# Kernel optimization log

Hardware: AMD Instinct MI355X
Metric: run time of the kernel (lower is better)

The kernel has to match this reference:

```python
import jax, jax.numpy as jnp
import numpy as np

B, S, H, D = 4, 2048, 16, 128

def setup_inputs() -> dict:
    key = jax.random.key(0)
    kq, kk, kv = jax.random.split(key, 3)
    shape = (B, S, H, D)
    return {
        "q": jax.random.normal(kq, shape, dtype=jnp.float32),
        "k": jax.random.normal(kk, shape, dtype=jnp.float32),
        "v": jax.random.normal(kv, shape, dtype=jnp.float32),
    }

def reference(q, k, v):
    # Fused recurrent linear attention (causal, unnormalized):
    #   H_t = H_{t-1} + k_t v_t^T ;  o_t = (scale * q_t) @ H_t
    scale = jnp.asarray(q.shape[-1], q.dtype) ** -0.5
    # move seq axis to front for scan: [S, B, H, D]
    qs = jnp.moveaxis(q, 1, 0) * scale
    ks = jnp.moveaxis(k, 1, 0)
    vs = jnp.moveaxis(v, 1, 0)

    def step(h, qkv):
        qt, kt, vt = qkv  # each [B, H, D]
        h = h + kt[..., :, None] * vt[..., None, :]  # [B, H, Dk, Dv]
        o = jnp.einsum('bhk,bhkv->bhv', qt, h)       # [B, H, Dv]
        return h, o

    h0 = jnp.zeros((q.shape[0], q.shape[2], q.shape[3], v.shape[3]), dtype=q.dtype)
    _, o = jax.lax.scan(step, h0, (qs, ks, vs))
    return jnp.moveaxis(o, 0, 1)  # [B, S, H, D]
```

## Files before the change

### kernel.cpp

```cpp
#include <hip/hip_runtime.h>


#define Bc 4
#define Sq 2048
#define Hh 16
#define Dd 128
#define RS (Hh * Dd)
#define Cc 128
#define NCH (Sq / Cc)
#define BHt (Bc * Hh)
#define NSEG 4
#define CPS (NCH / NSEG)
#define SCALE 0.08838834764831845f

using frag_ab = __attribute__((ext_vector_type(8))) short;
using frag_cd = __attribute__((ext_vector_type(4))) float;

__device__ __forceinline__ unsigned short f2bf(float f) {
  union { float f; unsigned u; } x; x.f = f;
  unsigned r = x.u + 0x7FFFu + ((x.u >> 16) & 1u);
  return (unsigned short)(r >> 16);
}
__device__ __forceinline__ float bf2f(unsigned short u) {
  union { unsigned u; float f; } x; x.u = ((unsigned)u) << 16;
  return x.f;
}
__device__ __forceinline__ int sw64(int r, int c) {
  return r * 64 + ((((c >> 3) ^ (r & 7)) << 3) | (c & 7));
}
__device__ __forceinline__ int sw128(int r, int c) {
  return r * 128 + ((((c >> 3) ^ (r & 15)) << 3) | (c & 7));
}
__device__ __forceinline__ int swKT(int dk, int t) {
  return dk * 128 + ((((t >> 3) ^ (dk ^ (dk >> 4))) & 15) << 3) + (t & 7);
}
__device__ __forceinline__ int swVT(int dv, int t) {
  return dv * 128 + ((((t >> 3) ^ dv) & 15) << 3) + (t & 7);
}

__global__ __launch_bounds__(256) void phA_state(const float* __restrict__ kg,
                                                 const float* __restrict__ vg,
                                                 unsigned short* __restrict__ st) {
  __shared__ unsigned short KT[128 * 128];
  __shared__ unsigned short VT[16 * 128];
  const int tid = threadIdx.x;
  const int bh = blockIdx.x & 63;
  const int slice = (blockIdx.x >> 6) & 7;
  const int seg = blockIdx.x >> 9;
  const int b = bh >> 4, h = bh & 15;
  const int dv0 = slice * 16;
  const size_t base = (size_t)b * Sq * RS + (size_t)h * Dd;
  const int w = tid >> 6, L = tid & 63, li = L & 15, q4 = L >> 4;
  const int kdk0 = (tid & 31) * 4;
  const int ktg4 = (tid >> 5) * 4;
  const int vdv0l = (tid & 3) * 4;
  const int vt0 = (tid >> 2) * 2;

  float4 rk[4][4];
  float4 rv[2];
  auto prefetch = [&](int n) {
    const size_t t0g = (size_t)n * Cc;
#pragma unroll
    for (int p = 0; p < 4; ++p) {
      const int t0 = p * 32 + ktg4;
#pragma unroll
      for (int i = 0; i < 4; ++i)
        rk[p][i] = *(const float4*)(kg + base + (t0g + t0 + i) * (size_t)RS + kdk0);
    }
#pragma unroll
    for (int i = 0; i < 2; ++i)
      rv[i] = *(const float4*)(vg + base + (t0g + vt0 + i) * (size_t)RS + dv0 + vdv0l);
  };

  frag_cd acc[2];
  acc[0] = (frag_cd){0.f, 0.f, 0.f, 0.f};
  acc[1] = (frag_cd){0.f, 0.f, 0.f, 0.f};
  const int n0 = seg * CPS;
  prefetch(n0);
  const size_t sbb = (size_t)bh * NCH * (128 * 128);

  auto store_acc = [&](int slot) {
    const size_t sb = sbb + (size_t)slot * (128 * 128);
#pragma unroll
    for (int nt = 0; nt < 2; ++nt)
#pragma unroll
      for (int r = 0; r < 4; ++r) {
        const int dv = dv0 + 4 * q4 + r;
        const int dk = 32 * w + 16 * nt + li;
        st[sb + (size_t)dv * 128 + dk] = f2bf(acc[nt][r]);
      }
  };

  for (int j = 0; j < CPS; ++j) {
    __syncthreads();
#pragma unroll
    for (int p = 0; p < 4; ++p) {
      const int t0 = p * 32 + ktg4;
#pragma unroll
      for (int jj = 0; jj < 4; ++jj) {
        ushort4 u;
        u.x = f2bf(((const float*)&rk[p][0])[jj]);
        u.y = f2bf(((const float*)&rk[p][1])[jj]);
        u.z = f2bf(((const float*)&rk[p][2])[jj]);
        u.w = f2bf(((const float*)&rk[p][3])[jj]);
        *(ushort4*)&KT[swKT(kdk0 + jj, t0)] = u;
      }
    }
#pragma unroll
    for (int jj = 0; jj < 4; ++jj) {
      ushort2 u;
      u.x = f2bf(((const float*)&rv[0])[jj]);
      u.y = f2bf(((const float*)&rv[1])[jj]);
      *(ushort2*)&VT[swVT(vdv0l + jj, vt0)] = u;
    }
    if (j + 1 < CPS) prefetch(n0 + j + 1);
    __syncthreads();
    if (j > 0) store_acc(n0 + j);
#pragma unroll
    for (int kt = 0; kt < 4; ++kt) {
      frag_ab af = *(const frag_ab*)&VT[swVT(li, 32 * kt + 8 * q4)];
#pragma unroll
      for (int nt = 0; nt < 2; ++nt) {
        frag_ab bf = *(const frag_ab*)&KT[swKT(32 * w + 16 * nt + li, 32 * kt + 8 * q4)];
        acc[nt] = __builtin_amdgcn_mfma_f32_16x16x32_bf16(af, bf, acc[nt], 0, 0, 0);
      }
    }
  }
  if (seg + 1 < NSEG) store_acc(n0);
}

__global__ __launch_bounds__(256) void phB_out(const float* __restrict__ qg,
                                               const float* __restrict__ kg,
                                               const float* __restrict__ vg,
                                               const unsigned short* __restrict__ st,
                                               float* __restrict__ o) {
  __shared__ unsigned short QP[128 * 128];
  __shared__ unsigned short Bb[128 * 64];
  const int tid = threadIdx.x;
  const int bid = blockIdx.x;
  const int bh = bid & 63, n = bid >> 6;
  const int b = bh >> 4, h = bh & 15;
  const size_t cbase = (size_t)b * Sq * RS + (size_t)n * Cc * RS + (size_t)h * Dd;
  const size_t sbh = (size_t)bh * NCH * (128 * 128);
  const int sseg = n >> 2, jj = n & 3;
  const int nmat = sseg + (jj ? 1 : 0);
  const int w = tid >> 6, L = tid & 63;
  const int wr = w >> 1, wc = w & 1, li = L & 15, q4 = L >> 4;

#pragma unroll
  for (int it = 0; it < 16; ++it) {
    const int f = it * 256 + tid;
    const int t = f >> 5;
    const int c0 = (f & 31) << 2;
    const float4 q4v = *(const float4*)(qg + cbase + (size_t)t * RS + c0);
    ushort4 qu;
    qu.x = f2bf(q4v.x * SCALE); qu.y = f2bf(q4v.y * SCALE);
    qu.z = f2bf(q4v.z * SCALE); qu.w = f2bf(q4v.w * SCALE);
    *(ushort4*)&QP[sw128(t, c0)] = qu;
  }
  frag_cd accO[4][4], accP[4][4];
#pragma unroll
  for (int i = 0; i < 4; ++i)
#pragma unroll
    for (int j = 0; j < 4; ++j) {
      accO[i][j] = (frag_cd){0.f, 0.f, 0.f, 0.f};
      accP[i][j] = (frag_cd){0.f, 0.f, 0.f, 0.f};
    }

  if (nmat > 0) {
    for (int half = 0; half < 2; ++half) {
      __syncthreads();
      if (nmat == 1) {
        const int slot = sseg ? 0 : n;
#pragma unroll
        for (int it = 0; it < 4; ++it) {
          const int f = it * 256 + tid;
          const int dv = f >> 3;
          const int c8 = (f & 7) << 3;
          const uint4 hv = *(const uint4*)(st + sbh + ((size_t)slot << 14) +
                                           (size_t)dv * 128 + 64 * half + c8);
          *(uint4*)&Bb[sw64(dv, c8)] = hv;
        }
      } else {
#pragma unroll
        for (int it = 0; it < 4; ++it) {
          const int f = it * 256 + tid;
          const int dv = f >> 3;
          const int c8 = (f & 7) << 3;
          float s8[8];
#pragma unroll
          for (int e = 0; e < 8; ++e) s8[e] = 0.f;
          for (int m = 0; m < nmat; ++m) {
            const int slot = (m < sseg) ? (m << 2) : n;
            const uint4 hv = *(const uint4*)(st + sbh + ((size_t)slot << 14) +
                                             (size_t)dv * 128 + 64 * half + c8);
            const unsigned hw[4] = {hv.x, hv.y, hv.z, hv.w};
#pragma unroll
            for (int e = 0; e < 4; ++e) {
              s8[2 * e + 0] += bf2f((unsigned short)(hw[e] & 0xFFFFu));
              s8[2 * e + 1] += bf2f((unsigned short)(hw[e] >> 16));
            }
          }
          unsigned pk[4];
#pragma unroll
          for (int e = 0; e < 4; ++e)
            pk[e] = (unsigned)f2bf(s8[2 * e]) | ((unsigned)f2bf(s8[2 * e + 1]) << 16);
          uint4 hv; hv.x = pk[0]; hv.y = pk[1]; hv.z = pk[2]; hv.w = pk[3];
          *(uint4*)&Bb[sw64(dv, c8)] = hv;
        }
      }
      __syncthreads();
#pragma unroll
      for (int kt = 0; kt < 2; ++kt) {
        const int ktg = 2 * half + kt;
        frag_ab af[4], bf_[4];
#pragma unroll
        for (int mt = 0; mt < 4; ++mt)
          af[mt] = *(const frag_ab*)&QP[sw128(64 * wr + 16 * mt + li, 32 * ktg + 8 * q4)];
#pragma unroll
        for (int nt = 0; nt < 4; ++nt)
          bf_[nt] = *(const frag_ab*)&Bb[sw64(64 * wc + 16 * nt + li, 32 * kt + 8 * q4)];
#pragma unroll
        for (int mt = 0; mt < 4; ++mt)
#pragma unroll
          for (int nt = 0; nt < 4; ++nt)
            accO[mt][nt] = __builtin_amdgcn_mfma_f32_16x16x32_bf16(af[mt], bf_[nt], accO[mt][nt], 0, 0, 0);
      }
    }
  }

  for (int half = 0; half < 2; ++half) {
    __syncthreads();
#pragma unroll
    for (int it = 0; it < 8; ++it) {
      const int f = it * 256 + tid;
      const int t = f >> 4;
      const int c0 = (f & 15) << 2;
      const float4 k4v = *(const float4*)(kg + cbase + (size_t)t * RS + 64 * half + c0);
      ushort4 ku;
      ku.x = f2bf(k4v.x); ku.y = f2bf(k4v.y); ku.z = f2bf(k4v.z); ku.w = f2bf(k4v.w);
      *(ushort4*)&Bb[sw64(t, c0)] = ku;
    }
    __syncthreads();
    if (64 * wc <= 64 * wr + 63) {
#pragma unroll
      for (int kt = 0; kt < 2; ++kt) {
        const int ktg = 2 * half + kt;
        frag_ab af[4], bf_[4];
#pragma unroll
        for (int mt = 0; mt < 4; ++mt)
          af[mt] = *(const frag_ab*)&QP[sw128(64 * wr + 16 * mt + li, 32 * ktg + 8 * q4)];
#pragma unroll
        for (int nt = 0; nt < 4; ++nt)
          bf_[nt] = *(const frag_ab*)&Bb[sw64(64 * wc + 16 * nt + li, 32 * kt + 8 * q4)];
#pragma unroll
        for (int mt = 0; mt < 4; ++mt)
#pragma unroll
          for (int nt = 0; nt < 4; ++nt)
            if (64 * wc + 16 * nt <= 64 * wr + 16 * mt + 15)
              accP[mt][nt] = __builtin_amdgcn_mfma_f32_16x16x32_bf16(af[mt], bf_[nt], accP[mt][nt], 0, 0, 0);
      }
    }
  }
  __syncthreads();
#pragma unroll
  for (int mt = 0; mt < 4; ++mt)
#pragma unroll
    for (int nt = 0; nt < 4; ++nt) {
      const int t0 = 64 * wr + 16 * mt + 4 * q4;
      const int s = 64 * wc + 16 * nt + li;
#pragma unroll
      for (int r = 0; r < 4; ++r) {
        const int t = t0 + r;
        QP[sw128(t, s)] = (s <= t) ? f2bf(accP[mt][nt][r]) : (unsigned short)0;
      }
    }

  for (int half = 0; half < 2; ++half) {
    __syncthreads();
#pragma unroll
    for (int it = 0; it < 8; ++it) {
      const int sl = (tid & 15) | ((it & 3) << 4);
      const int c0 = ((tid >> 4) | ((it >> 2) << 4)) << 2;
      const int s = 64 * half + sl;
      const float4 v4v = *(const float4*)(vg + cbase + (size_t)s * RS + c0);
      Bb[sw64(c0 + 0, sl)] = f2bf(v4v.x);
      Bb[sw64(c0 + 1, sl)] = f2bf(v4v.y);
      Bb[sw64(c0 + 2, sl)] = f2bf(v4v.z);
      Bb[sw64(c0 + 3, sl)] = f2bf(v4v.w);
    }
    __syncthreads();
#pragma unroll
    for (int kt = 0; kt < 2; ++kt) {
      const int ktg = 2 * half + kt;
      if (32 * ktg > 64 * wr + 63) continue;
      frag_ab af[4], bf_[4];
#pragma unroll
      for (int mt = 0; mt < 4; ++mt)
        af[mt] = *(const frag_ab*)&QP[sw128(64 * wr + 16 * mt + li, 32 * ktg + 8 * q4)];
#pragma unroll
      for (int nt = 0; nt < 4; ++nt)
        bf_[nt] = *(const frag_ab*)&Bb[sw64(64 * wc + 16 * nt + li, 32 * kt + 8 * q4)];
#pragma unroll
      for (int mt = 0; mt < 4; ++mt)
#pragma unroll
        for (int nt = 0; nt < 4; ++nt)
          if (32 * ktg <= 64 * wr + 16 * mt + 15)
            accO[mt][nt] = __builtin_amdgcn_mfma_f32_16x16x32_bf16(af[mt], bf_[nt], accO[mt][nt], 0, 0, 0);
    }
  }
#pragma unroll
  for (int mt = 0; mt < 4; ++mt)
#pragma unroll
    for (int nt = 0; nt < 4; ++nt)
#pragma unroll
      for (int r = 0; r < 4; ++r) {
        const int t = 64 * wr + 16 * mt + 4 * q4 + r;
        const int dv = 64 * wc + 16 * nt + li;
        o[cbase + (size_t)t * RS + dv] = accO[mt][nt][r];
      }
}

extern "C" void kernel_launch(void* const* d_in, const int* in_sizes, int n_in,
                              void* d_out, int out_size, void* d_ws, size_t ws_size,
                              hipStream_t stream) {
  const float* q = (const float*)d_in[0];
  const float* k = (const float*)d_in[1];
  const float* v = (const float*)d_in[2];
  float* o = (float*)d_out;
  unsigned short* st = (unsigned short*)d_ws;
  hipLaunchKernelGGL(phA_state, dim3(BHt * 8 * NSEG), dim3(256), 0, stream, k, v, st);
  hipLaunchKernelGGL(phB_out, dim3(BHt * NCH), dim3(256), 0, stream, q, k, v, st, o);
}
```

Measured before the change: 289.4 us.

## Split phB output chunk into two 64-row query tiles per block

Each phB block now handles 64 query rows of a 128-token chunk instead of 128, doubling the grid and halving the accumulator registers and Q shared memory. A launch-bounds occupancy hint of 4 blocks per CU is added. The first tile skips loading the later K rows and the second half of V because of causality. The cost is that the inter-chunk state matrix and the K/V data are loaded and converted twice per chunk, once by each tile block.

```diff
diff --git a/kernel.cpp b/kernel.cpp
--- a/kernel.cpp
+++ b/kernel.cpp
@@ -129,18 +129,19 @@
   if (seg + 1 < NSEG) store_acc(n0);
 }
 
-__global__ __launch_bounds__(256) void phB_out(const float* __restrict__ qg,
-                                               const float* __restrict__ kg,
-                                               const float* __restrict__ vg,
-                                               const unsigned short* __restrict__ st,
-                                               float* __restrict__ o) {
-  __shared__ unsigned short QP[128 * 128];
+__global__ __launch_bounds__(256, 4) void phB_out(const float* __restrict__ qg,
+                                                  const float* __restrict__ kg,
+                                                  const float* __restrict__ vg,
+                                                  const unsigned short* __restrict__ st,
+                                                  float* __restrict__ o) {
+  __shared__ unsigned short QP[64 * 128];
   __shared__ unsigned short Bb[128 * 64];
   const int tid = threadIdx.x;
   const int bid = blockIdx.x;
-  const int bh = bid & 63, n = bid >> 6;
+  const int bh = bid & 63, n = (bid >> 6) & 15, tb = bid >> 10;
   const int b = bh >> 4, h = bh & 15;
   const size_t cbase = (size_t)b * Sq * RS + (size_t)n * Cc * RS + (size_t)h * Dd;
+  const size_t tbase = cbase + (size_t)(64 * tb) * RS;
   const size_t sbh = (size_t)bh * NCH * (128 * 128);
   const int sseg = n >> 2, jj = n & 3;
   const int nmat = sseg + (jj ? 1 : 0);
@@ -148,19 +149,19 @@
   const int wr = w >> 1, wc = w & 1, li = L & 15, q4 = L >> 4;
 
 #pragma unroll
-  for (int it = 0; it < 16; ++it) {
+  for (int it = 0; it < 8; ++it) {
     const int f = it * 256 + tid;
     const int t = f >> 5;
     const int c0 = (f & 31) << 2;
-    const float4 q4v = *(const float4*)(qg + cbase + (size_t)t * RS + c0);
+    const float4 q4v = *(const float4*)(qg + tbase + (size_t)t * RS + c0);
     ushort4 qu;
     qu.x = f2bf(q4v.x * SCALE); qu.y = f2bf(q4v.y * SCALE);
     qu.z = f2bf(q4v.z * SCALE); qu.w = f2bf(q4v.w * SCALE);
     *(ushort4*)&QP[sw128(t, c0)] = qu;
   }
-  frag_cd accO[4][4], accP[4][4];
-#pragma unroll
-  for (int i = 0; i < 4; ++i)
+  frag_cd accO[2][4], accP[2][4];
+#pragma unroll
+  for (int i = 0; i < 2; ++i)
 #pragma unroll
     for (int j = 0; j < 4; ++j) {
       accO[i][j] = (frag_cd){0.f, 0.f, 0.f, 0.f};
@@ -213,15 +214,15 @@
 #pragma unroll
       for (int kt = 0; kt < 2; ++kt) {
         const int ktg = 2 * half + kt;
-        frag_ab af[4], bf_[4];
-#pragma unroll
-        for (int mt = 0; mt < 4; ++mt)
-          af[mt] = *(const frag_ab*)&QP[sw128(64 * wr + 16 * mt + li, 32 * ktg + 8 * q4)];
+        frag_ab af[2], bf_[4];
+#pragma unroll
+        for (int mt = 0; mt < 2; ++mt)
+          af[mt] = *(const frag_ab*)&QP[sw128(32 * wr + 16 * mt + li, 32 * ktg + 8 * q4)];
 #pragma unroll
         for (int nt = 0; nt < 4; ++nt)
           bf_[nt] = *(const frag_ab*)&Bb[sw64(64 * wc + 16 * nt + li, 32 * kt + 8 * q4)];
 #pragma unroll
-        for (int mt = 0; mt < 4; ++mt)
+        for (int mt = 0; mt < 2; ++mt)
 #pragma unroll
           for (int nt = 0; nt < 4; ++nt)
             accO[mt][nt] = __builtin_amdgcn_mfma_f32_16x16x32_bf16(af[mt], bf_[nt], accO[mt][nt], 0, 0, 0);
@@ -231,52 +232,66 @@
 
   for (int half = 0; half < 2; ++half) {
     __syncthreads();
-#pragma unroll
-    for (int it = 0; it < 8; ++it) {
-      const int f = it * 256 + tid;
-      const int t = f >> 4;
-      const int c0 = (f & 15) << 2;
-      const float4 k4v = *(const float4*)(kg + cbase + (size_t)t * RS + 64 * half + c0);
-      ushort4 ku;
-      ku.x = f2bf(k4v.x); ku.y = f2bf(k4v.y); ku.z = f2bf(k4v.z); ku.w = f2bf(k4v.w);
-      *(ushort4*)&Bb[sw64(t, c0)] = ku;
-    }
-    __syncthreads();
-    if (64 * wc <= 64 * wr + 63) {
+    if (tb) {
+#pragma unroll
+      for (int it = 0; it < 8; ++it) {
+        const int f = it * 256 + tid;
+        const int t = f >> 4;
+        const int c0 = (f & 15) << 2;
+        const float4 k4v = *(const float4*)(kg + cbase + (size_t)t * RS + 64 * half + c0);
+        ushort4 ku;
+        ku.x = f2bf(k4v.x); ku.y = f2bf(k4v.y); ku.z = f2bf(k4v.z); ku.w = f2bf(k4v.w);
+        *(ushort4*)&Bb[sw64(t, c0)] = ku;
+      }
+    } else {
+#pragma unroll
+      for (int it = 0; it < 4; ++it) {
+        const int f = it * 256 + tid;
+        const int t = f >> 4;
+        const int c0 = (f & 15) << 2;
+        const float4 k4v = *(const float4*)(kg + cbase + (size_t)t * RS + 64 * half + c0);
+        ushort4 ku;
+        ku.x = f2bf(k4v.x); ku.y = f2bf(k4v.y); ku.z = f2bf(k4v.z); ku.w = f2bf(k4v.w);
+        *(ushort4*)&Bb[sw64(t, c0)] = ku;
+      }
+    }
+    __syncthreads();
+    if (64 * wc <= 64 * tb + 32 * wr + 31) {
 #pragma unroll
       for (int kt = 0; kt < 2; ++kt) {
         const int ktg = 2 * half + kt;
-        frag_ab af[4], bf_[4];
-#pragma unroll
-        for (int mt = 0; mt < 4; ++mt)
-          af[mt] = *(const frag_ab*)&QP[sw128(64 * wr + 16 * mt + li, 32 * ktg + 8 * q4)];
+        frag_ab af[2], bf_[4];
+#pragma unroll
+        for (int mt = 0; mt < 2; ++mt)
+          af[mt] = *(const frag_ab*)&QP[sw128(32 * wr + 16 * mt + li, 32 * ktg + 8 * q4)];
 #pragma unroll
         for (int nt = 0; nt < 4; ++nt)
           bf_[nt] = *(const frag_ab*)&Bb[sw64(64 * wc + 16 * nt + li, 32 * kt + 8 * q4)];
 #pragma unroll
-        for (int mt = 0; mt < 4; ++mt)
+        for (int mt = 0; mt < 2; ++mt)
 #pragma unroll
           for (int nt = 0; nt < 4; ++nt)
-            if (64 * wc + 16 * nt <= 64 * wr + 16 * mt + 15)
+            if (64 * wc + 16 * nt <= 64 * tb + 32 * wr + 16 * mt + 15)
               accP[mt][nt] = __builtin_amdgcn_mfma_f32_16x16x32_bf16(af[mt], bf_[nt], accP[mt][nt], 0, 0, 0);
       }
     }
   }
   __syncthreads();
 #pragma unroll
-  for (int mt = 0; mt < 4; ++mt)
+  for (int mt = 0; mt < 2; ++mt)
 #pragma unroll
     for (int nt = 0; nt < 4; ++nt) {
-      const int t0 = 64 * wr + 16 * mt + 4 * q4;
+      const int t0 = 32 * wr + 16 * mt + 4 * q4;
       const int s = 64 * wc + 16 * nt + li;
 #pragma unroll
       for (int r = 0; r < 4; ++r) {
         const int t = t0 + r;
-        QP[sw128(t, s)] = (s <= t) ? f2bf(accP[mt][nt][r]) : (unsigned short)0;
-      }
-    }
-
-  for (int half = 0; half < 2; ++half) {
+        QP[sw128(t, s)] = (s <= t + 64 * tb) ? f2bf(accP[mt][nt][r]) : (unsigned short)0;
+      }
+    }
+
+  const int nh2 = tb ? 2 : 1;
+  for (int half = 0; half < nh2; ++half) {
     __syncthreads();
 #pragma unroll
     for (int it = 0; it < 8; ++it) {
@@ -293,31 +308,31 @@
 #pragma unroll
     for (int kt = 0; kt < 2; ++kt) {
       const int ktg = 2 * half + kt;
-      if (32 * ktg > 64 * wr + 63) continue;
-      frag_ab af[4], bf_[4];
-#pragma unroll
-      for (int mt = 0; mt < 4; ++mt)
-        af[mt] = *(const frag_ab*)&QP[sw128(64 * wr + 16 * mt + li, 32 * ktg + 8 * q4)];
+      if (32 * ktg > 64 * tb + 32 * wr + 31) continue;
+      frag_ab af[2], bf_[4];
+#pragma unroll
+      for (int mt = 0; mt < 2; ++mt)
+        af[mt] = *(const frag_ab*)&QP[sw128(32 * wr + 16 * mt + li, 32 * ktg + 8 * q4)];
 #pragma unroll
       for (int nt = 0; nt < 4; ++nt)
         bf_[nt] = *(const frag_ab*)&Bb[sw64(64 * wc + 16 * nt + li, 32 * kt + 8 * q4)];
 #pragma unroll
-      for (int mt = 0; mt < 4; ++mt)
+      for (int mt = 0; mt < 2; ++mt)
 #pragma unroll
         for (int nt = 0; nt < 4; ++nt)
-          if (32 * ktg <= 64 * wr + 16 * mt + 15)
+          if (32 * ktg <= 64 * tb + 32 * wr + 16 * mt + 15)
             accO[mt][nt] = __builtin_amdgcn_mfma_f32_16x16x32_bf16(af[mt], bf_[nt], accO[mt][nt], 0, 0, 0);
     }
   }
 #pragma unroll
-  for (int mt = 0; mt < 4; ++mt)
+  for (int mt = 0; mt < 2; ++mt)
 #pragma unroll
     for (int nt = 0; nt < 4; ++nt)
 #pragma unroll
       for (int r = 0; r < 4; ++r) {
-        const int t = 64 * wr + 16 * mt + 4 * q4 + r;
+        const int t = 32 * wr + 16 * mt + 4 * q4 + r;
         const int dv = 64 * wc + 16 * nt + li;
-        o[cbase + (size_t)t * RS + dv] = accO[mt][nt][r];
+        o[tbase + (size_t)t * RS + dv] = accO[mt][nt][r];
       }
 }
 
@@ -330,5 +345,5 @@
   float* o = (float*)d_out;
   unsigned short* st = (unsigned short*)d_ws;
   hipLaunchKernelGGL(phA_state, dim3(BHt * 8 * NSEG), dim3(256), 0, stream, k, v, st);
-  hipLaunchKernelGGL(phB_out, dim3(BHt * NCH), dim3(256), 0, stream, q, k, v, st, o);
-}
+  hipLaunchKernelGGL(phB_out, dim3(BHt * NCH * 2), dim3(256), 0, stream, q, k, v, st, o);
+}
```

Measured after the change: 284.0 us. No clear change (-1.9%).

## Halve state segments and add a fixup kernel combining segment prefix states

Applied to the files above, without the earlier changes.

Sequence segments for the chunked state computation drop from four to two. A new small kernel adds the first segment's final state into each second-segment chunk state, so the output kernel reads a single precomputed state matrix instead of summing several on the fly. The output kernel's block index mapping also changes so that consecutive blocks share the same batch-head. This trades less parallelism in the state phase, with longer serial chains per segment, plus an extra launch and state-memory pass for simpler, lighter loads in the output phase.

```diff
diff --git a/kernel.cpp b/kernel.cpp
--- a/kernel.cpp
+++ b/kernel.cpp
@@ -9,7 +9,7 @@
 #define Cc 128
 #define NCH (Sq / Cc)
 #define BHt (Bc * Hh)
-#define NSEG 4
+#define NSEG 2
 #define CPS (NCH / NSEG)
 #define SCALE 0.08838834764831845f
 
@@ -129,6 +129,37 @@
   if (seg + 1 < NSEG) store_acc(n0);
 }
 
+__global__ __launch_bounds__(256) void phFix(unsigned short* __restrict__ st) {
+  const int bh = blockIdx.x & 63, n8 = blockIdx.x >> 6;
+  const int n = 8 + n8;
+  const int tid = threadIdx.x;
+  const size_t b0 = ((size_t)(bh * NCH + 0)) << 14;
+  const size_t bn = ((size_t)(bh * NCH + n)) << 14;
+#pragma unroll
+  for (int i = 0; i < 8; ++i) {
+    const size_t off = (size_t)i * 2048 + tid * 8;
+    const uint4 t0 = *(const uint4*)(st + b0 + off);
+    if (n8 == 0) {
+      *(uint4*)(st + bn + off) = t0;
+    } else {
+      const uint4 ln = *(const uint4*)(st + bn + off);
+      const unsigned a[4] = {ln.x, ln.y, ln.z, ln.w};
+      const unsigned c[4] = {t0.x, t0.y, t0.z, t0.w};
+      unsigned pk[4];
+#pragma unroll
+      for (int e = 0; e < 4; ++e) {
+        const float lo = bf2f((unsigned short)(a[e] & 0xFFFFu)) +
+                         bf2f((unsigned short)(c[e] & 0xFFFFu));
+        const float hi = bf2f((unsigned short)(a[e] >> 16)) +
+                         bf2f((unsigned short)(c[e] >> 16));
+        pk[e] = (unsigned)f2bf(lo) | ((unsigned)f2bf(hi) << 16);
+      }
+      uint4 out; out.x = pk[0]; out.y = pk[1]; out.z = pk[2]; out.w = pk[3];
+      *(uint4*)(st + bn + off) = out;
+    }
+  }
+}
+
 __global__ __launch_bounds__(256) void phB_out(const float* __restrict__ qg,
                                                const float* __restrict__ kg,
                                                const float* __restrict__ vg,
@@ -138,12 +169,10 @@
   __shared__ unsigned short Bb[128 * 64];
   const int tid = threadIdx.x;
   const int bid = blockIdx.x;
-  const int bh = bid & 63, n = bid >> 6;
+  const int bh = bid >> 4, n = bid & 15;
   const int b = bh >> 4, h = bh & 15;
   const size_t cbase = (size_t)b * Sq * RS + (size_t)n * Cc * RS + (size_t)h * Dd;
-  const size_t sbh = (size_t)bh * NCH * (128 * 128);
-  const int sseg = n >> 2, jj = n & 3;
-  const int nmat = sseg + (jj ? 1 : 0);
+  const size_t sb = (size_t)(bh * 16 + n) * (128 * 128);
   const int w = tid >> 6, L = tid & 63;
   const int wr = w >> 1, wc = w & 1, li = L & 15, q4 = L >> 4;
 
@@ -167,47 +196,16 @@
       accP[i][j] = (frag_cd){0.f, 0.f, 0.f, 0.f};
     }
 
-  if (nmat > 0) {
+  if (n) {
     for (int half = 0; half < 2; ++half) {
       __syncthreads();
-      if (nmat == 1) {
-        const int slot = sseg ? 0 : n;
-#pragma unroll
-        for (int it = 0; it < 4; ++it) {
-          const int f = it * 256 + tid;
-          const int dv = f >> 3;
-          const int c8 = (f & 7) << 3;
-          const uint4 hv = *(const uint4*)(st + sbh + ((size_t)slot << 14) +
-                                           (size_t)dv * 128 + 64 * half + c8);
-          *(uint4*)&Bb[sw64(dv, c8)] = hv;
-        }
-      } else {
-#pragma unroll
-        for (int it = 0; it < 4; ++it) {
-          const int f = it * 256 + tid;
-          const int dv = f >> 3;
-          const int c8 = (f & 7) << 3;
-          float s8[8];
-#pragma unroll
-          for (int e = 0; e < 8; ++e) s8[e] = 0.f;
-          for (int m = 0; m < nmat; ++m) {
-            const int slot = (m < sseg) ? (m << 2) : n;
-            const uint4 hv = *(const uint4*)(st + sbh + ((size_t)slot << 14) +
-                                             (size_t)dv * 128 + 64 * half + c8);
-            const unsigned hw[4] = {hv.x, hv.y, hv.z, hv.w};
-#pragma unroll
-            for (int e = 0; e < 4; ++e) {
-              s8[2 * e + 0] += bf2f((unsigned short)(hw[e] & 0xFFFFu));
-              s8[2 * e + 1] += bf2f((unsigned short)(hw[e] >> 16));
-            }
-          }
-          unsigned pk[4];
-#pragma unroll
-          for (int e = 0; e < 4; ++e)
-            pk[e] = (unsigned)f2bf(s8[2 * e]) | ((unsigned)f2bf(s8[2 * e + 1]) << 16);
-          uint4 hv; hv.x = pk[0]; hv.y = pk[1]; hv.z = pk[2]; hv.w = pk[3];
-          *(uint4*)&Bb[sw64(dv, c8)] = hv;
-        }
+#pragma unroll
+      for (int it = 0; it < 4; ++it) {
+        const int f = it * 256 + tid;
+        const int dv = f >> 3;
+        const int c8 = (f & 7) << 3;
+        const uint4 hv = *(const uint4*)(st + sb + (size_t)dv * 128 + 64 * half + c8);
+        *(uint4*)&Bb[sw64(dv, c8)] = hv;
       }
       __syncthreads();
 #pragma unroll
@@ -330,5 +328,6 @@
   float* o = (float*)d_out;
   unsigned short* st = (unsigned short*)d_ws;
   hipLaunchKernelGGL(phA_state, dim3(BHt * 8 * NSEG), dim3(256), 0, stream, k, v, st);
+  hipLaunchKernelGGL(phFix, dim3(BHt * 8), dim3(256), 0, stream, st);
   hipLaunchKernelGGL(phB_out, dim3(BHt * NCH), dim3(256), 0, stream, q, k, v, st, o);
 }
```

After: 286.4 us. Within noise of the previous version (-1.0%).
